# Optimization experiments

Measured on AMD Instinct MI355X. Metric: run time of the kernel, lower is better.

The kernel has to match this reference:

```python
import jax, jax.numpy as jnp
import numpy as np


def _batched_histc(x, bins):
    # x: [N, ...] -> per-sample histogram over [0, 1], matching torch.histc semantics:
    # bin = floor(v * bins), v == 1.0 goes to last bin, values outside [0,1] ignored.
    N = x.shape[0]
    flat = x.reshape(N, -1)
    idx = jnp.clip((flat * bins).astype(jnp.int32), 0, bins - 1)  # [N, P]
    valid = ((flat >= 0.0) & (flat <= 1.0)).astype(x.dtype)
    gidx = (jnp.arange(N, dtype=jnp.int32)[:, None] * bins + idx).reshape(-1)
    counts = jax.ops.segment_sum(valid.reshape(-1), gidx, num_segments=N * bins)
    return counts.reshape(N, bins)


def _mlp(h, W1, b1, W2, b2, W3, b3, W4, b4):
    h = jax.nn.relu(h @ W1 + b1)
    h = jax.nn.relu(h @ W2 + b2)
    h = jax.nn.relu(h @ W3 + b3)
    return h @ W4 + b4  # [N, 1]


def setup_inputs() -> dict:
    key = jax.random.key(0)
    ks = jax.random.split(key, 5)
    bins = 128
    N, C, H, W = 128, 1, 1024, 1024
    x = jax.random.uniform(ks[0], (N, C, H, W), dtype=jnp.float32)
    def lin(k, fan_in, fan_out):
        s = 1.0 / np.sqrt(fan_in)
        return jax.random.uniform(k, (fan_in, fan_out), jnp.float32, -s, s)
    return {
        "x": x,
        "W1": lin(ks[1], bins, 32), "b1": jnp.zeros((32,), jnp.float32),
        "W2": lin(ks[2], 32, 64),   "b2": jnp.zeros((64,), jnp.float32),
        "W3": lin(ks[3], 64, 128),  "b3": jnp.zeros((128,), jnp.float32),
        "W4": lin(ks[4], 128, 1),   "b4": jnp.zeros((1,), jnp.float32),
        "bins": bins,
    }


def reference(x, W1, b1, W2, b2, W3, b3, W4, b4, bins):
    hst = _batched_histc(x, bins)                       # [N, bins]
    w = _mlp(hst, W1, b1, W2, b2, W3, b3, W4, b4)       # [N, 1]
    w = w[:, :, None, None]                             # [N, 1, 1, 1]
    return x * w
```

## Files before the change

### kernel.cpp

```cpp
#include <hip/hip_runtime.h>

#define N_IMG 128
#define BINS 128
#define HW_ELEMS (1 << 20)
#define CHUNKS 16
#define NCOPY 16
#define HPAD 132

typedef float f32x4 __attribute__((ext_vector_type(4)));

__global__ __launch_bounds__(256) void hist_kernel(const float* __restrict__ x,
                                                   int* __restrict__ parthist) {
    __shared__ int lh[NCOPY * HPAD];
    const int tid = threadIdx.x;
    const int cpy = tid >> 4;

    for (int i = tid; i < NCOPY * HPAD; i += 256) lh[i] = 0;
    __syncthreads();

    const int blk   = blockIdx.x;
    const int img   = blk / CHUNKS;
    const int chunk = blk % CHUNKS;
    const int chunk_elems = HW_ELEMS / CHUNKS;
    const long long base = (long long)img * HW_ELEMS + (long long)chunk * chunk_elems;
    const f32x4* xv = (const f32x4*)(x + base);
    const int n4 = chunk_elems / 4;

    int* myh = &lh[cpy * HPAD];

    for (int i = tid; i < n4; i += 256) {
        f32x4 v = xv[i];
        #pragma unroll
        for (int k = 0; k < 4; ++k) {
            float f = v[k];
            if (f >= 0.0f && f <= 1.0f) {
                int b = (int)(f * (float)BINS);
                b = b > (BINS - 1) ? (BINS - 1) : b;
                atomicAdd(&myh[b], 1);
            }
        }
    }
    __syncthreads();

    if (tid < BINS) {
        int s = 0;
        #pragma unroll
        for (int c = 0; c < NCOPY; ++c) s += lh[c * HPAD + tid];
        parthist[blk * BINS + tid] = s;
    }
}

__global__ __launch_bounds__(128) void mlp_kernel(const int* __restrict__ parthist,
                                                  const float* __restrict__ W1, const float* __restrict__ b1,
                                                  const float* __restrict__ W2, const float* __restrict__ b2,
                                                  const float* __restrict__ W3, const float* __restrict__ b3,
                                                  const float* __restrict__ W4, const float* __restrict__ b4,
                                                  float* __restrict__ wout) {
    __shared__ float h0[128], a1[32], a2[64], a3[128];
    const int img = blockIdx.x;
    const int t   = threadIdx.x;

    {
        int s = 0;
        #pragma unroll
        for (int c = 0; c < CHUNKS; ++c)
            s += parthist[(img * CHUNKS + c) * BINS + t];
        h0[t] = (float)s;
    }
    __syncthreads();

    if (t < 32) {
        float acc = b1[t];
        #pragma unroll 8
        for (int i = 0; i < 128; ++i) acc += h0[i] * W1[i * 32 + t];
        a1[t] = fmaxf(acc, 0.0f);
    }
    __syncthreads();

    if (t < 64) {
        float acc = b2[t];
        #pragma unroll 8
        for (int i = 0; i < 32; ++i) acc += a1[i] * W2[i * 64 + t];
        a2[t] = fmaxf(acc, 0.0f);
    }
    __syncthreads();

    {
        float acc = b3[t];
        #pragma unroll 8
        for (int i = 0; i < 64; ++i) acc += a2[i] * W3[i * 128 + t];
        a3[t] = fmaxf(acc, 0.0f);
    }
    __syncthreads();

    if (t == 0) {
        float acc = b4[0];
        for (int i = 0; i < 128; ++i) acc += a3[i] * W4[i];
        wout[img] = acc;
    }
}

__global__ __launch_bounds__(256) void scale_kernel(const float* __restrict__ x,
                                                    const float* __restrict__ w,
                                                    float* __restrict__ out,
                                                    long long n4) {
    const long long stride = (long long)gridDim.x * blockDim.x;
    const f32x4* xv = (const f32x4*)x;
    f32x4* ov = (f32x4*)out;
    for (long long i = (long long)blockIdx.x * blockDim.x + threadIdx.x; i < n4; i += stride) {
        int img = (int)(i >> 18);
        float s = w[img];
        f32x4 v = xv[i];
        v *= s;
        __builtin_nontemporal_store(v, &ov[i]);
    }
}

extern "C" void kernel_launch(void* const* d_in, const int* in_sizes, int n_in,
                              void* d_out, int out_size, void* d_ws, size_t ws_size,
                              hipStream_t stream) {
    const float* x  = (const float*)d_in[0];
    const float* W1 = (const float*)d_in[1];
    const float* b1 = (const float*)d_in[2];
    const float* W2 = (const float*)d_in[3];
    const float* b2 = (const float*)d_in[4];
    const float* W3 = (const float*)d_in[5];
    const float* b3 = (const float*)d_in[6];
    const float* W4 = (const float*)d_in[7];
    const float* b4 = (const float*)d_in[8];

    int*   parthist = (int*)d_ws;
    float* wout = (float*)((char*)d_ws + (size_t)N_IMG * CHUNKS * BINS * sizeof(int));

    hist_kernel<<<N_IMG * CHUNKS, 256, 0, stream>>>(x, parthist);

    mlp_kernel<<<N_IMG, 128, 0, stream>>>(parthist, W1, b1, W2, b2, W3, b3, W4, b4, wout);

    const long long n4 = (long long)N_IMG * HW_ELEMS / 4;
    scale_kernel<<<8192, 256, 0, stream>>>(x, wout, (float*)d_out, n4);
}
```

Before: 311.3 us.

## Fuse MLP into histogram via last-block counter and batch hist/scale for cache reuse

The MLP is folded into the histogram kernel: the last chunk block for each image, detected with an atomic counter, reduces the partial histograms and runs the MLP. Work is split into batches of 32 images, alternating histogram and scale kernels, so the re-read of x in the scale pass can hit the last-level cache. This removes a separate MLP launch and the full second DRAM read of x. In exchange it adds a memset, more launches, kernel tail effects per batch, and atomic ordering between blocks.

```diff
diff --git a/kernel.cpp b/kernel.cpp
--- a/kernel.cpp
+++ b/kernel.cpp
@@ -3,116 +3,130 @@
 #define N_IMG 128
 #define BINS 128
 #define HW_ELEMS (1 << 20)
-#define CHUNKS 16
+#define BATCH_IMGS 32
+#define NBATCH (N_IMG / BATCH_IMGS)
+#define CHUNKS 32
+#define CHUNK_ELEMS (HW_ELEMS / CHUNKS)
 #define NCOPY 16
 #define HPAD 132
 
 typedef float f32x4 __attribute__((ext_vector_type(4)));
 
-__global__ __launch_bounds__(256) void hist_kernel(const float* __restrict__ x,
-                                                   int* __restrict__ parthist) {
-    __shared__ int lh[NCOPY * HPAD];
-    const int tid = threadIdx.x;
-    const int cpy = tid >> 4;
+__device__ __forceinline__ int rmw_inc(int* p) {
+    return __hip_atomic_fetch_add(p, 1, __ATOMIC_RELAXED, __HIP_MEMORY_SCOPE_AGENT);
+}
+__device__ __forceinline__ void ag_store(int* p, int v) {
+    __hip_atomic_store(p, v, __ATOMIC_RELAXED, __HIP_MEMORY_SCOPE_AGENT);
+}
+__device__ __forceinline__ int ag_load(const int* p) {
+    return __hip_atomic_load(p, __ATOMIC_RELAXED, __HIP_MEMORY_SCOPE_AGENT);
+}
+__device__ __forceinline__ void ag_store_f(float* p, float v) {
+    __hip_atomic_store(p, v, __ATOMIC_RELAXED, __HIP_MEMORY_SCOPE_AGENT);
+}
 
-    for (int i = tid; i < NCOPY * HPAD; i += 256) lh[i] = 0;
+__global__ __launch_bounds__(256) void hist_mlp_kernel(
+    const float* __restrict__ x,
+    const float* __restrict__ W1, const float* __restrict__ b1,
+    const float* __restrict__ W2, const float* __restrict__ b2,
+    const float* __restrict__ W3, const float* __restrict__ b3,
+    const float* __restrict__ W4, const float* __restrict__ b4,
+    int* __restrict__ parthist, int* __restrict__ done,
+    float* __restrict__ wout, int img_base)
+{
+    __shared__ int   lh[NCOPY * HPAD];
+    __shared__ float h0[BINS], a1[32], a2[64], a3[BINS];
+    __shared__ int   retsh;
+
+    const int t     = threadIdx.x;
+    const int cpy   = t >> 4;
+    const int img   = img_base + (blockIdx.x >> 5);
+    const int chunk = blockIdx.x & (CHUNKS - 1);
+
+    for (int i = t; i < NCOPY * HPAD; i += 256) lh[i] = 0;
     __syncthreads();
 
-    const int blk   = blockIdx.x;
-    const int img   = blk / CHUNKS;
-    const int chunk = blk % CHUNKS;
-    const int chunk_elems = HW_ELEMS / CHUNKS;
-    const long long base = (long long)img * HW_ELEMS + (long long)chunk * chunk_elems;
-    const f32x4* xv = (const f32x4*)(x + base);
-    const int n4 = chunk_elems / 4;
-
-    int* myh = &lh[cpy * HPAD];
-
-    for (int i = tid; i < n4; i += 256) {
-        f32x4 v = xv[i];
+    const f32x4* src = (const f32x4*)(x + (size_t)img * HW_ELEMS
+                                        + (size_t)chunk * CHUNK_ELEMS);
+    const int n4 = CHUNK_ELEMS / 4;
+    for (int i = t; i < n4; i += 256) {
+        f32x4 v = src[i];
         #pragma unroll
         for (int k = 0; k < 4; ++k) {
             float f = v[k];
             if (f >= 0.0f && f <= 1.0f) {
-                int b = (int)(f * (float)BINS);
-                b = b > (BINS - 1) ? (BINS - 1) : b;
-                atomicAdd(&myh[b], 1);
+                int b = (int)(f * 128.0f);
+                b = b > 127 ? 127 : b;
+                atomicAdd(&lh[cpy * HPAD + b], 1);
             }
         }
     }
     __syncthreads();
 
-    if (tid < BINS) {
+    if (t < BINS) {
         int s = 0;
         #pragma unroll
-        for (int c = 0; c < NCOPY; ++c) s += lh[c * HPAD + tid];
-        parthist[blk * BINS + tid] = s;
+        for (int c = 0; c < NCOPY; ++c) s += lh[c * HPAD + t];
+        ag_store(&parthist[((size_t)img * CHUNKS + chunk) * BINS + t], s);
+    }
+    __syncthreads();
+    if (t == 0) retsh = rmw_inc(&done[img]);
+    __syncthreads();
+
+    if (retsh == CHUNKS - 1) {
+        if (t < BINS) {
+            int s = 0;
+            #pragma unroll 8
+            for (int c = 0; c < CHUNKS; ++c)
+                s += ag_load(&parthist[((size_t)img * CHUNKS + c) * BINS + t]);
+            h0[t] = (float)s;
+        }
+        __syncthreads();
+        if (t < 32) {
+            float acc = b1[t];
+            #pragma unroll 8
+            for (int i = 0; i < 128; ++i) acc += h0[i] * W1[i * 32 + t];
+            a1[t] = fmaxf(acc, 0.0f);
+        }
+        __syncthreads();
+        if (t < 64) {
+            float acc = b2[t];
+            #pragma unroll 8
+            for (int i = 0; i < 32; ++i) acc += a1[i] * W2[i * 64 + t];
+            a2[t] = fmaxf(acc, 0.0f);
+        }
+        __syncthreads();
+        if (t < 128) {
+            float acc = b3[t];
+            #pragma unroll 8
+            for (int i = 0; i < 64; ++i) acc += a2[i] * W3[i * 128 + t];
+            a3[t] = fmaxf(acc, 0.0f);
+        }
+        __syncthreads();
+        if (t < 64) {
+            float p = a3[t] * W4[t] + a3[t + 64] * W4[t + 64];
+            #pragma unroll
+            for (int off = 32; off > 0; off >>= 1)
+                p += __shfl_down(p, off, 64);
+            if (t == 0) ag_store_f(&wout[img], p + b4[0]);
+        }
     }
 }
 
-__global__ __launch_bounds__(128) void mlp_kernel(const int* __restrict__ parthist,
-                                                  const float* __restrict__ W1, const float* __restrict__ b1,
-                                                  const float* __restrict__ W2, const float* __restrict__ b2,
-                                                  const float* __restrict__ W3, const float* __restrict__ b3,
-                                                  const float* __restrict__ W4, const float* __restrict__ b4,
-                                                  float* __restrict__ wout) {
-    __shared__ float h0[128], a1[32], a2[64], a3[128];
-    const int img = blockIdx.x;
-    const int t   = threadIdx.x;
-
-    {
-        int s = 0;
-        #pragma unroll
-        for (int c = 0; c < CHUNKS; ++c)
-            s += parthist[(img * CHUNKS + c) * BINS + t];
-        h0[t] = (float)s;
-    }
-    __syncthreads();
-
-    if (t < 32) {
-        float acc = b1[t];
-        #pragma unroll 8
-        for (int i = 0; i < 128; ++i) acc += h0[i] * W1[i * 32 + t];
-        a1[t] = fmaxf(acc, 0.0f);
-    }
-    __syncthreads();
-
-    if (t < 64) {
-        float acc = b2[t];
-        #pragma unroll 8
-        for (int i = 0; i < 32; ++i) acc += a1[i] * W2[i * 64 + t];
-        a2[t] = fmaxf(acc, 0.0f);
-    }
-    __syncthreads();
-
-    {
-        float acc = b3[t];
-        #pragma unroll 8
-        for (int i = 0; i < 64; ++i) acc += a2[i] * W3[i * 128 + t];
-        a3[t] = fmaxf(acc, 0.0f);
-    }
-    __syncthreads();
-
-    if (t == 0) {
-        float acc = b4[0];
-        for (int i = 0; i < 128; ++i) acc += a3[i] * W4[i];
-        wout[img] = acc;
-    }
-}
-
-__global__ __launch_bounds__(256) void scale_kernel(const float* __restrict__ x,
-                                                    const float* __restrict__ w,
-                                                    float* __restrict__ out,
-                                                    long long n4) {
+__global__ __launch_bounds__(256) void scale_kernel(
+    const float* __restrict__ x, const float* __restrict__ w,
+    float* __restrict__ out, long long base4, long long n4)
+{
     const long long stride = (long long)gridDim.x * blockDim.x;
     const f32x4* xv = (const f32x4*)x;
     f32x4* ov = (f32x4*)out;
-    for (long long i = (long long)blockIdx.x * blockDim.x + threadIdx.x; i < n4; i += stride) {
-        int img = (int)(i >> 18);
-        float s = w[img];
-        f32x4 v = xv[i];
+    for (long long i = (long long)blockIdx.x * blockDim.x + threadIdx.x;
+         i < n4; i += stride) {
+        long long gi = base4 + i;
+        float s = w[(int)(gi >> 18)];
+        f32x4 v = xv[gi];
         v *= s;
-        __builtin_nontemporal_store(v, &ov[i]);
+        __builtin_nontemporal_store(v, &ov[gi]);
     }
 }
 
@@ -129,13 +143,18 @@
     const float* W4 = (const float*)d_in[7];
     const float* b4 = (const float*)d_in[8];
 
-    int*   parthist = (int*)d_ws;
-    float* wout = (float*)((char*)d_ws + (size_t)N_IMG * CHUNKS * BINS * sizeof(int));
+    int*   done     = (int*)d_ws;
+    int*   parthist = done + N_IMG;
+    float* wout     = (float*)(parthist + (size_t)N_IMG * CHUNKS * BINS);
 
-    hist_kernel<<<N_IMG * CHUNKS, 256, 0, stream>>>(x, parthist);
+    hipMemsetAsync(done, 0, N_IMG * sizeof(int), stream);
 
-    mlp_kernel<<<N_IMG, 128, 0, stream>>>(parthist, W1, b1, W2, b2, W3, b3, W4, b4, wout);
-
-    const long long n4 = (long long)N_IMG * HW_ELEMS / 4;
-    scale_kernel<<<8192, 256, 0, stream>>>(x, wout, (float*)d_out, n4);
+    const long long batch4 = (long long)BATCH_IMGS * HW_ELEMS / 4;
+    for (int b = 0; b < NBATCH; ++b) {
+        hist_mlp_kernel<<<BATCH_IMGS * CHUNKS, 256, 0, stream>>>(
+            x, W1, b1, W2, b2, W3, b3, W4, b4,
+            parthist, done, wout, b * BATCH_IMGS);
+        scale_kernel<<<2048, 256, 0, stream>>>(
+            x, wout, (float*)d_out, (long long)b * batch4, batch4);
+    }
 }
```

Result: slower. 351.0 us (+12.7%).
